# Performance work log

Hardware: AMD Instinct MI355X
Metric: run time of the kernel (lower is better)

Reference implementation:

```python
import jax, jax.numpy as jnp
import numpy as np

N_NODES = 50000
N_EDGES = 625000
IN_DIM = 512
HID = 128
OUT_DIM = 40
N_LAYERS = 3


def setup_inputs() -> dict:
    key = jax.random.key(0)
    ks = jax.random.split(key, 12)
    features = jax.random.normal(ks[0], (N_NODES, IN_DIM), dtype=jnp.float32)
    src = jax.random.randint(ks[1], (N_EDGES,), 0, N_NODES, dtype=jnp.int32)
    dst = jax.random.randint(ks[2], (N_EDGES,), 0, N_NODES, dtype=jnp.int32)
    edge_w = jax.random.uniform(ks[3], (N_EDGES,), dtype=jnp.float32)
    s_in = 1.0 / np.sqrt(IN_DIM)
    s_h = 1.0 / np.sqrt(HID)
    emb_W = jax.random.uniform(ks[4], (IN_DIM, HID), jnp.float32, -s_in, s_in)
    emb_b = jax.random.uniform(ks[5], (HID,), jnp.float32, -s_in, s_in)
    W1 = jax.random.uniform(ks[6], (N_LAYERS, HID, HID), jnp.float32, -s_h, s_h)
    b1 = jax.random.uniform(ks[7], (N_LAYERS, HID), jnp.float32, -s_h, s_h)
    W2 = jax.random.uniform(ks[8], (N_LAYERS, HID, HID), jnp.float32, -s_h, s_h)
    b2 = jax.random.uniform(ks[9], (N_LAYERS, HID), jnp.float32, -s_h, s_h)
    ro_W = jax.random.uniform(ks[10], (HID, OUT_DIM), jnp.float32, -s_h, s_h)
    ro_b = jax.random.uniform(ks[11], (OUT_DIM,), jnp.float32, -s_h, s_h)
    return {"features": features, "src": src, "dst": dst, "edge_w": edge_w,
            "emb_W": emb_W, "emb_b": emb_b, "W1": W1, "b1": b1,
            "W2": W2, "b2": b2, "ro_W": ro_W, "ro_b": ro_b}


def reference(features, src, dst, edge_w, emb_W, emb_b, W1, b1, W2, b2, ro_W, ro_b):
    # Input embedding: [N, in_dim] -> [N, hid]
    h = features @ emb_W + emb_b
    n = h.shape[0]
    for l in range(N_LAYERS):
        # GINConv (sum aggregator, eps=0): agg_i = sum_{(u->i)} w * h_u
        msg = h[src] * edge_w[:, None]                      # [E, hid]
        agg = jax.ops.segment_sum(msg, dst, num_segments=n)  # [N, hid]
        z = h + agg                                          # (1+eps)*h + agg
        # apply_func MLP: Linear -> ReLU -> Linear, then outer ReLU
        z = jax.nn.relu(z @ W1[l] + b1[l]) @ W2[l] + b2[l]
        h = jax.nn.relu(z)
    return h @ ro_W + ro_b
```

## Files before the change

### kernel.cpp

```cpp
#include <hip/hip_runtime.h>

#define NN 50000
#define NE 625000
#define IND 512
#define HID 128
#define OUTD 40
#define NL 3
#define NB 196

typedef short v8s __attribute__((ext_vector_type(8)));
typedef float v4f __attribute__((ext_vector_type(4)));
typedef const __attribute__((address_space(1))) unsigned int gu32;
typedef __attribute__((address_space(3))) unsigned int lu32;

#define MFMA __builtin_amdgcn_mfma_f32_16x16x32_bf16

__device__ inline ushort f2bf(float x) {
    unsigned u = __float_as_uint(x);
    u += 0x7FFF + ((u >> 16) & 1);
    return (ushort)(u >> 16);
}
__device__ inline float bf2f(ushort b) { return __uint_as_float(((unsigned)b) << 16); }

__device__ inline void split8(float4 a, float4 b, v8s& hi, v8s& lo) {
    float v[8] = {a.x, a.y, a.z, a.w, b.x, b.y, b.z, b.w};
    v8s h, l;
#pragma unroll
    for (int i = 0; i < 8; i++) {
        ushort hu = f2bf(v[i]);
        h[i] = (short)hu;
        l[i] = (short)f2bf(v[i] - bf2f(hu));
    }
    hi = h;
    lo = l;
}

template <int NI>
__device__ inline void stage(const ushort* __restrict__ g, ushort* l, int tid) {
    const int wid = tid >> 6;
#pragma unroll
    for (int j = 0; j < NI; j++) {
        __builtin_amdgcn_global_load_lds(
            (gu32*)((const char*)g + (size_t)(j * 256 + tid) * 16),
            (lu32*)((char*)l + (j * 256 + (wid << 6)) * 16), 16, 0, 0);
    }
}


__global__ __launch_bounds__(256) void count_kernel(const int* __restrict__ dst,
                                                    int* __restrict__ deg) {
    int e = blockIdx.x * 256 + threadIdx.x;
    if (e < NE) atomicAdd(&deg[dst[e]], 1);
}

__global__ __launch_bounds__(256) void scan1(const int* __restrict__ deg,
                                             int* __restrict__ ex,
                                             int* __restrict__ bsum) {
    __shared__ int s[256];
    int t = threadIdx.x;
    int idx = blockIdx.x * 256 + t;
    int d = idx < NN ? deg[idx] : 0;
    s[t] = d;
    __syncthreads();
#pragma unroll
    for (int off = 1; off < 256; off <<= 1) {
        int v = (t >= off) ? s[t - off] : 0;
        __syncthreads();
        s[t] += v;
        __syncthreads();
    }
    if (idx < NN) ex[idx] = s[t] - d;
    if (t == 255) bsum[blockIdx.x] = s[255];
}

__global__ __launch_bounds__(256) void scan2(const int* __restrict__ bsum,
                                             int* __restrict__ bpre) {
    __shared__ int s[256];
    int t = threadIdx.x;
    int d = t < NB ? bsum[t] : 0;
    s[t] = d;
    __syncthreads();
#pragma unroll
    for (int off = 1; off < 256; off <<= 1) {
        int v = (t >= off) ? s[t - off] : 0;
        __syncthreads();
        s[t] += v;
        __syncthreads();
    }
    if (t < NB) bpre[t] = s[t] - d;
}

__global__ __launch_bounds__(256) void scan3(const int* __restrict__ deg,
                                             const int* __restrict__ ex,
                                             const int* __restrict__ bpre,
                                             int* __restrict__ rp,
                                             int* __restrict__ cursor) {
    int idx = blockIdx.x * 256 + threadIdx.x;
    if (idx < NN) {
        int v = ex[idx] + bpre[blockIdx.x];
        rp[idx] = v;
        cursor[idx] = v;
        if (idx == NN - 1) rp[NN] = v + deg[idx];
    }
}

__global__ __launch_bounds__(256) void fill_kernel(const int* __restrict__ src,
                                                   const int* __restrict__ dst,
                                                   const float* __restrict__ ew,
                                                   int* __restrict__ cursor,
                                                   int2* __restrict__ csr) {
    int e = blockIdx.x * 256 + threadIdx.x;
    if (e < NE) {
        int d = dst[e];
        int pos = atomicAdd(&cursor[d], 1);
        csr[pos] = make_int2(src[e], __float_as_int(ew[e]));
    }
}


__global__ __launch_bounds__(256) void conv_emb(const float* __restrict__ W,
                                                ushort* __restrict__ P) {
    int idx = blockIdx.x * 256 + threadIdx.x;
    int k = idx >> 7;
    int c = idx & 127;
    float v = W[(size_t)k * HID + c];
    ushort hb = f2bf(v);
    ushort lb = f2bf(v - bf2f(hb));
    int it = k >> 6, kl = k & 63;
    int pos = it * 16384 + c * 64 + (kl ^ ((c & 7) << 3));
    P[pos] = hb;
    P[pos + 8192] = lb;
}

__global__ __launch_bounds__(256) void conv_mlp(const float* __restrict__ W1,
                                                const float* __restrict__ W2,
                                                ushort* __restrict__ P) {
    int idx = blockIdx.x * 256 + threadIdx.x;
    int lg = idx >> 14;
    int r = idx & 16383;
    int k = r >> 7, c = r & 127;
    int l = lg >> 1, g = lg & 1;
    const float* src = (g ? W2 : W1) + (size_t)l * HID * HID;
    float v = src[(size_t)k * HID + c];
    ushort hb = f2bf(v);
    ushort lb = f2bf(v - bf2f(hb));
    int q = c >> 5, cl = c & 31;
    int pos = lg * 32768 + q * 8192 + cl * 128 + (k ^ ((c & 7) << 3));
    P[pos] = hb;
    P[pos + 4096] = lb;
}

__global__ __launch_bounds__(256) void conv_ro(const float* __restrict__ W,
                                               ushort* __restrict__ Th,
                                               ushort* __restrict__ Tl) {
    int idx = blockIdx.x * 256 + threadIdx.x;
    int c = idx >> 7;
    int kk = idx & 127;
    float v = (c < OUTD) ? W[(size_t)kk * OUTD + c] : 0.f;
    ushort h = f2bf(v);
    Th[idx] = h;
    Tl[idx] = f2bf(v - bf2f(h));
}


__global__ __launch_bounds__(256) void emb_mfma(const float* __restrict__ X,
                                                const ushort* __restrict__ Wp,
                                                const float* __restrict__ B,
                                                float* __restrict__ H) {
    __shared__ __align__(16) ushort Wb[2][16384];
    const int tid = threadIdx.x;
    const int wid = tid >> 6, lane = tid & 63;
    const int lane15 = lane & 15, kg = (lane >> 4) * 8;
    const int swc = (lane15 & 7) << 3;
    const int brow = blockIdx.x * 64;
    const int grow = brow + wid * 16 + lane15;
    const float* xr = X + (size_t)(grow < NN ? grow : 0) * IND + kg;

    v4f acc[8];
#pragma unroll
    for (int i = 0; i < 8; i++) acc[i] = (v4f)0.f;

    float4 x0 = *reinterpret_cast<const float4*>(xr);
    float4 x1 = *reinterpret_cast<const float4*>(xr + 4);
    float4 x2 = *reinterpret_cast<const float4*>(xr + 32);
    float4 x3 = *reinterpret_cast<const float4*>(xr + 36);
    stage<8>(Wp, &Wb[0][0], tid);

    for (int it = 0; it < 8; ++it) {
        float4 n0, n1, n2, n3;
        if (it < 7) {
            const float* xn = xr + (it + 1) * 64;
            n0 = *reinterpret_cast<const float4*>(xn);
            n1 = *reinterpret_cast<const float4*>(xn + 4);
            n2 = *reinterpret_cast<const float4*>(xn + 32);
            n3 = *reinterpret_cast<const float4*>(xn + 36);
            stage<8>(Wp + (size_t)(it + 1) * 16384, &Wb[(it + 1) & 1][0], tid);
            asm volatile("s_waitcnt vmcnt(12)" ::: "memory");
        } else {
            asm volatile("s_waitcnt vmcnt(0)" ::: "memory");
        }
        __builtin_amdgcn_s_barrier();
        v8s ah0, al0, ah1, al1;
        split8(x0, x1, ah0, al0);
        split8(x2, x3, ah1, al1);
        const ushort* cb = &Wb[it & 1][0];
        const int s0 = kg ^ swc;
        const int s1 = (32 + kg) ^ swc;
        __builtin_amdgcn_s_setprio(1);
#pragma unroll
        for (int nf = 0; nf < 8; nf++) {
            int rb = (nf * 16 + lane15) * 64;
            v8s bh0 = *reinterpret_cast<const v8s*>(&cb[rb + s0]);
            v8s bl0 = *reinterpret_cast<const v8s*>(&cb[8192 + rb + s0]);
            v8s bh1 = *reinterpret_cast<const v8s*>(&cb[rb + s1]);
            v8s bl1 = *reinterpret_cast<const v8s*>(&cb[8192 + rb + s1]);
            v4f a = acc[nf];
            a = MFMA(ah0, bh0, a, 0, 0, 0);
            a = MFMA(al0, bh0, a, 0, 0, 0);
            a = MFMA(ah0, bl0, a, 0, 0, 0);
            a = MFMA(ah1, bh1, a, 0, 0, 0);
            a = MFMA(al1, bh1, a, 0, 0, 0);
            a = MFMA(ah1, bl1, a, 0, 0, 0);
            acc[nf] = a;
        }
        __builtin_amdgcn_s_setprio(0);
        asm volatile("s_waitcnt lgkmcnt(0)" ::: "memory");
        __builtin_amdgcn_s_barrier();
        x0 = n0; x1 = n1; x2 = n2; x3 = n3;
    }
#pragma unroll
    for (int nf = 0; nf < 8; nf++) {
        int col = nf * 16 + lane15;
        float bias = B[col];
#pragma unroll
        for (int r = 0; r < 4; r++) {
            int g = brow + wid * 16 + (lane >> 4) * 4 + r;
            if (g < NN) H[(size_t)g * HID + col] = acc[nf][r] + bias;
        }
    }
}


__global__ __launch_bounds__(256) void agg_kernel(const float* __restrict__ h,
                                                  const int* __restrict__ rp,
                                                  const int2* __restrict__ csr,
                                                  float* __restrict__ z) {
    const int node = blockIdx.x * 8 + (threadIdx.x >> 5);
    const int c4 = (threadIdx.x & 31) << 2;
    const float* hp = h + c4;
    v4f a0 = *reinterpret_cast<const v4f*>(hp + (size_t)node * HID);
    v4f a1 = (v4f)0.f, a2 = (v4f)0.f, a3 = (v4f)0.f;
    int k = rp[node];
    const int ke = rp[node + 1];
    for (; k + 3 < ke; k += 4) {
        int2 e0 = csr[k], e1 = csr[k + 1], e2 = csr[k + 2], e3 = csr[k + 3];
        a0 += __int_as_float(e0.y) * *reinterpret_cast<const v4f*>(hp + (size_t)e0.x * HID);
        a1 += __int_as_float(e1.y) * *reinterpret_cast<const v4f*>(hp + (size_t)e1.x * HID);
        a2 += __int_as_float(e2.y) * *reinterpret_cast<const v4f*>(hp + (size_t)e2.x * HID);
        a3 += __int_as_float(e3.y) * *reinterpret_cast<const v4f*>(hp + (size_t)e3.x * HID);
    }
    for (; k < ke; k++) {
        int2 e = csr[k];
        a0 += __int_as_float(e.y) * *reinterpret_cast<const v4f*>(hp + (size_t)e.x * HID);
    }
    *reinterpret_cast<v4f*>(z + (size_t)node * HID + c4) = (a0 + a1) + (a2 + a3);
}


template <int LAST>
__global__ __launch_bounds__(256) void mlp_mfma(const float* __restrict__ Z,
                                                const ushort* __restrict__ Wlp,
                                                const float* __restrict__ B1,
                                                const float* __restrict__ B2,
                                                const ushort* __restrict__ RWh,
                                                const ushort* __restrict__ RWl,
                                                const float* __restrict__ RB,
                                                float* __restrict__ H,
                                                float* __restrict__ OUT) {
    __shared__ __align__(16) ushort Wb[2][8192];
    __shared__ __align__(16) ushort Hh[64 * 128];
    __shared__ __align__(16) ushort Hl[64 * 128];
    const int tid = threadIdx.x;
    const int wid = tid >> 6, lane = tid & 63;
    const int lane15 = lane & 15, kg = (lane >> 4) * 8;
    const int swc = (lane15 & 7) << 3;
    const int brow = blockIdx.x * 64;
    const int grow = brow + wid * 16 + lane15;
    const int rowl = wid * 16 + lane15;
    const int sw = (rowl & 7) << 3;

    const float* zr = Z + (size_t)(grow < NN ? grow : 0) * HID + kg;
    float4 za[4], zb[4];
#pragma unroll
    for (int ks = 0; ks < 4; ks++) {
        za[ks] = *reinterpret_cast<const float4*>(zr + ks * 32);
        zb[ks] = *reinterpret_cast<const float4*>(zr + ks * 32 + 4);
    }
    stage<4>(Wlp, &Wb[0][0], tid);

    v8s ah[4], al[4];
    v4f acc[8];
#pragma unroll
    for (int i = 0; i < 8; i++) acc[i] = (v4f)0.f;

    for (int q = 0; q < 8; q++) {
        if (q < 7) {
            stage<4>(Wlp + (size_t)(q + 1) * 8192, &Wb[(q + 1) & 1][0], tid);
            asm volatile("s_waitcnt vmcnt(4)" ::: "memory");
        } else {
            asm volatile("s_waitcnt vmcnt(0)" ::: "memory");
        }
        __builtin_amdgcn_s_barrier();
        if (q == 0) {
#pragma unroll
            for (int ks = 0; ks < 4; ks++) split8(za[ks], zb[ks], ah[ks], al[ks]);
        }
        if (q == 4) {
#pragma unroll
            for (int ks = 0; ks < 4; ks++) {
                int idx = rowl * 128 + ((ks * 32 + kg) ^ sw);
                ah[ks] = *reinterpret_cast<const v8s*>(&Hh[idx]);
                al[ks] = *reinterpret_cast<const v8s*>(&Hl[idx]);
            }
        }
        const ushort* cb = &Wb[q & 1][0];
        const int nfb = (q & 3) * 2;
        __builtin_amdgcn_s_setprio(1);
#pragma unroll
        for (int t = 0; t < 2; t++) {
            int rb = (t * 16 + lane15) * 128;
            v4f a = acc[nfb + t];
#pragma unroll
            for (int ks = 0; ks < 4; ks++) {
                int s = (ks * 32 + kg) ^ swc;
                v8s bh = *reinterpret_cast<const v8s*>(&cb[rb + s]);
                v8s bl = *reinterpret_cast<const v8s*>(&cb[4096 + rb + s]);
                a = MFMA(ah[ks], bh, a, 0, 0, 0);
                a = MFMA(al[ks], bh, a, 0, 0, 0);
                a = MFMA(ah[ks], bl, a, 0, 0, 0);
            }
            acc[nfb + t] = a;
        }
        __builtin_amdgcn_s_setprio(0);
        if (q < 4) {
#pragma unroll
            for (int t = 0; t < 2; t++) {
                int nf = nfb + t;
                int col = nf * 16 + lane15;
                float b = B1[col];
#pragma unroll
                for (int r = 0; r < 4; r++) {
                    int rl2 = wid * 16 + (lane >> 4) * 4 + r;
                    float v = acc[nf][r] + b;
                    v = v > 0.f ? v : 0.f;
                    ushort hb = f2bf(v);
                    int idx = rl2 * 128 + (col ^ ((rl2 & 7) << 3));
                    Hh[idx] = hb;
                    Hl[idx] = f2bf(v - bf2f(hb));
                }
                acc[nf] = (v4f)0.f;
            }
        } else if (LAST == 0) {
#pragma unroll
            for (int t = 0; t < 2; t++) {
                int nf = nfb + t;
                int col = nf * 16 + lane15;
                float b = B2[col];
#pragma unroll
                for (int r = 0; r < 4; r++) {
                    int g = brow + wid * 16 + (lane >> 4) * 4 + r;
                    if (g < NN) H[(size_t)g * HID + col] = fmaxf(acc[nf][r] + b, 0.f);
                }
            }
        } else {
#pragma unroll
            for (int t = 0; t < 2; t++) {
                int nf = nfb + t;
                int col = nf * 16 + lane15;
                float b = B2[col];
#pragma unroll
                for (int r = 0; r < 4; r++) {
                    int rl2 = wid * 16 + (lane >> 4) * 4 + r;
                    float v = fmaxf(acc[nf][r] + b, 0.f);
                    ushort hb = f2bf(v);
                    int idx = rl2 * 128 + (col ^ ((rl2 & 7) << 3));
                    Hh[idx] = hb;
                    Hl[idx] = f2bf(v - bf2f(hb));
                }
            }
        }
        asm volatile("s_waitcnt lgkmcnt(0)" ::: "memory");
        __builtin_amdgcn_s_barrier();
    }

    if (LAST) {
#pragma unroll
        for (int ks = 0; ks < 4; ks++) {
            int idx = rowl * 128 + ((ks * 32 + kg) ^ sw);
            ah[ks] = *reinterpret_cast<const v8s*>(&Hh[idx]);
            al[ks] = *reinterpret_cast<const v8s*>(&Hl[idx]);
        }
        v4f a3[3];
#pragma unroll
        for (int i = 0; i < 3; i++) a3[i] = (v4f)0.f;
#pragma unroll
        for (int nf = 0; nf < 3; nf++) {
            const ushort* bp = RWh + (size_t)(nf * 16 + lane15) * HID + kg;
            const ushort* bq = RWl + (size_t)(nf * 16 + lane15) * HID + kg;
            v4f a = a3[nf];
#pragma unroll
            for (int ks = 0; ks < 4; ks++) {
                v8s bh = *reinterpret_cast<const v8s*>(bp + ks * 32);
                v8s bl = *reinterpret_cast<const v8s*>(bq + ks * 32);
                a = MFMA(ah[ks], bh, a, 0, 0, 0);
                a = MFMA(al[ks], bh, a, 0, 0, 0);
                a = MFMA(ah[ks], bl, a, 0, 0, 0);
            }
            a3[nf] = a;
        }
#pragma unroll
        for (int nf = 0; nf < 3; nf++) {
            int col = nf * 16 + lane15;
            if (col < OUTD) {
                float b = RB[col];
#pragma unroll
                for (int r = 0; r < 4; r++) {
                    int g = brow + wid * 16 + (lane >> 4) * 4 + r;
                    if (g < NN) OUT[(size_t)g * OUTD + col] = a3[nf][r] + b;
                }
            }
        }
    }
}


extern "C" void kernel_launch(void* const* d_in, const int* in_sizes, int n_in,
                              void* d_out, int out_size, void* d_ws, size_t ws_size,
                              hipStream_t stream) {
    const float* features = (const float*)d_in[0];
    const int* src = (const int*)d_in[1];
    const int* dst = (const int*)d_in[2];
    const float* ew = (const float*)d_in[3];
    const float* embW = (const float*)d_in[4];
    const float* embB = (const float*)d_in[5];
    const float* W1 = (const float*)d_in[6];
    const float* B1 = (const float*)d_in[7];
    const float* W2 = (const float*)d_in[8];
    const float* B2 = (const float*)d_in[9];
    const float* roW = (const float*)d_in[10];
    const float* roB = (const float*)d_in[11];
    float* out = (float*)d_out;

    float* h = (float*)d_ws;
    float* z = h + (size_t)NN * HID;
    int* rp = (int*)(z + (size_t)NN * HID);
    int2* csr = (int2*)(rp + NN + 16);
    int* cursor = (int*)(csr + NE);
    int* deg = cursor + NN;
    int* ex = deg + NN;
    int* bsum = ex + NN;
    int* bpre = bsum + NB + 4;
    ushort* Wemb_p = (ushort*)(bpre + NB + 4);
    ushort* Wmlp_p = Wemb_p + 8 * 16384;
    ushort* roWt_h = Wmlp_p + (size_t)NL * 8 * 8192;
    ushort* roWt_l = roWt_h + 48 * 128;

    conv_emb<<<256, 256, 0, stream>>>(embW, Wemb_p);
    conv_mlp<<<384, 256, 0, stream>>>(W1, W2, Wmlp_p);
    conv_ro<<<24, 256, 0, stream>>>(roW, roWt_h, roWt_l);

    hipMemsetAsync(deg, 0, NN * sizeof(int), stream);
    count_kernel<<<(NE + 255) / 256, 256, 0, stream>>>(dst, deg);
    scan1<<<NB, 256, 0, stream>>>(deg, ex, bsum);
    scan2<<<1, 256, 0, stream>>>(bsum, bpre);
    scan3<<<NB, 256, 0, stream>>>(deg, ex, bpre, rp, cursor);
    fill_kernel<<<(NE + 255) / 256, 256, 0, stream>>>(src, dst, ew, cursor, csr);

    emb_mfma<<<(NN + 63) / 64, 256, 0, stream>>>(features, Wemb_p, embB, h);

    for (int l = 0; l < NL; l++) {
        agg_kernel<<<NN / 8, 256, 0, stream>>>(h, rp, csr, z);
        const ushort* wl = Wmlp_p + (size_t)l * 8 * 8192;
        const float* b1 = B1 + (size_t)l * HID;
        const float* b2 = B2 + (size_t)l * HID;
        if (l < NL - 1) {
            mlp_mfma<0><<<(NN + 63) / 64, 256, 0, stream>>>(
                z, wl, b1, b2, roWt_h, roWt_l, roB, h, out);
        } else {
            mlp_mfma<1><<<(NN + 63) / 64, 256, 0, stream>>>(
                z, wl, b1, b2, roWt_h, roWt_l, roB, h, out);
        }
    }
}
```

Baseline: 539.8 us.

## Enlarge embedding blocks, triple-buffer MLP weights, unroll aggregation gathers by eight

The embedding GEMM now runs 512-thread blocks covering 128 rows, so each staged weight tile is shared by twice as many rows and fewer loads go out per thread. The MLP kernel moves from double to triple buffering of weight chunks, prefetching two stages ahead, and fully unrolls the stage loop. The aggregation loop issues eight neighbor gathers before accumulating, to expose more memory parallelism. The trade is more LDS per block in the MLP, larger blocks in the embedding, and higher register pressure in aggregation, all of which can lower occupancy.

```diff
diff --git a/kernel.cpp b/kernel.cpp
--- a/kernel.cpp
+++ b/kernel.cpp
@@ -35,14 +35,14 @@
     lo = l;
 }
 
-template <int NI>
+template <int NI, int NT>
 __device__ inline void stage(const ushort* __restrict__ g, ushort* l, int tid) {
-    const int wid = tid >> 6;
+    const int wbase = tid & ~63;
 #pragma unroll
     for (int j = 0; j < NI; j++) {
         __builtin_amdgcn_global_load_lds(
-            (gu32*)((const char*)g + (size_t)(j * 256 + tid) * 16),
-            (lu32*)((char*)l + (j * 256 + (wid << 6)) * 16), 16, 0, 0);
+            (gu32*)((const char*)g + (size_t)(j * NT + tid) * 16),
+            (lu32*)((char*)l + (j * NT + wbase) * 16), 16, 0, 0);
     }
 }
 
@@ -163,7 +163,7 @@
 }
 
 
-__global__ __launch_bounds__(256) void emb_mfma(const float* __restrict__ X,
+__global__ __launch_bounds__(512) void emb_mfma(const float* __restrict__ X,
                                                 const ushort* __restrict__ Wp,
                                                 const float* __restrict__ B,
                                                 float* __restrict__ H) {
@@ -172,7 +172,7 @@
     const int wid = tid >> 6, lane = tid & 63;
     const int lane15 = lane & 15, kg = (lane >> 4) * 8;
     const int swc = (lane15 & 7) << 3;
-    const int brow = blockIdx.x * 64;
+    const int brow = blockIdx.x * 128;
     const int grow = brow + wid * 16 + lane15;
     const float* xr = X + (size_t)(grow < NN ? grow : 0) * IND + kg;
 
@@ -184,7 +184,7 @@
     float4 x1 = *reinterpret_cast<const float4*>(xr + 4);
     float4 x2 = *reinterpret_cast<const float4*>(xr + 32);
     float4 x3 = *reinterpret_cast<const float4*>(xr + 36);
-    stage<8>(Wp, &Wb[0][0], tid);
+    stage<4, 512>(Wp, &Wb[0][0], tid);
 
     for (int it = 0; it < 8; ++it) {
         float4 n0, n1, n2, n3;
@@ -194,8 +194,8 @@
             n1 = *reinterpret_cast<const float4*>(xn + 4);
             n2 = *reinterpret_cast<const float4*>(xn + 32);
             n3 = *reinterpret_cast<const float4*>(xn + 36);
-            stage<8>(Wp + (size_t)(it + 1) * 16384, &Wb[(it + 1) & 1][0], tid);
-            asm volatile("s_waitcnt vmcnt(12)" ::: "memory");
+            stage<4, 512>(Wp + (size_t)(it + 1) * 16384, &Wb[(it + 1) & 1][0], tid);
+            asm volatile("s_waitcnt vmcnt(8)" ::: "memory");
         } else {
             asm volatile("s_waitcnt vmcnt(0)" ::: "memory");
         }
@@ -252,14 +252,32 @@
     v4f a1 = (v4f)0.f, a2 = (v4f)0.f, a3 = (v4f)0.f;
     int k = rp[node];
     const int ke = rp[node + 1];
-    for (; k + 3 < ke; k += 4) {
+    for (; k + 7 < ke; k += 8) {
         int2 e0 = csr[k], e1 = csr[k + 1], e2 = csr[k + 2], e3 = csr[k + 3];
+        int2 e4 = csr[k + 4], e5 = csr[k + 5], e6 = csr[k + 6], e7 = csr[k + 7];
+        const v4f v0 = *reinterpret_cast<const v4f*>(hp + (size_t)e0.x * HID);
+        const v4f v1 = *reinterpret_cast<const v4f*>(hp + (size_t)e1.x * HID);
+        const v4f v2 = *reinterpret_cast<const v4f*>(hp + (size_t)e2.x * HID);
+        const v4f v3 = *reinterpret_cast<const v4f*>(hp + (size_t)e3.x * HID);
+        const v4f v4 = *reinterpret_cast<const v4f*>(hp + (size_t)e4.x * HID);
+        const v4f v5 = *reinterpret_cast<const v4f*>(hp + (size_t)e5.x * HID);
+        const v4f v6 = *reinterpret_cast<const v4f*>(hp + (size_t)e6.x * HID);
+        const v4f v7 = *reinterpret_cast<const v4f*>(hp + (size_t)e7.x * HID);
+        a0 += __int_as_float(e0.y) * v0;
+        a1 += __int_as_float(e1.y) * v1;
+        a2 += __int_as_float(e2.y) * v2;
+        a3 += __int_as_float(e3.y) * v3;
+        a0 += __int_as_float(e4.y) * v4;
+        a1 += __int_as_float(e5.y) * v5;
+        a2 += __int_as_float(e6.y) * v6;
+        a3 += __int_as_float(e7.y) * v7;
+    }
+    for (; k + 1 < ke; k += 2) {
+        int2 e0 = csr[k], e1 = csr[k + 1];
         a0 += __int_as_float(e0.y) * *reinterpret_cast<const v4f*>(hp + (size_t)e0.x * HID);
         a1 += __int_as_float(e1.y) * *reinterpret_cast<const v4f*>(hp + (size_t)e1.x * HID);
-        a2 += __int_as_float(e2.y) * *reinterpret_cast<const v4f*>(hp + (size_t)e2.x * HID);
-        a3 += __int_as_float(e3.y) * *reinterpret_cast<const v4f*>(hp + (size_t)e3.x * HID);
-    }
-    for (; k < ke; k++) {
+    }
+    if (k < ke) {
         int2 e = csr[k];
         a0 += __int_as_float(e.y) * *reinterpret_cast<const v4f*>(hp + (size_t)e.x * HID);
     }
@@ -277,7 +295,7 @@
                                                 const float* __restrict__ RB,
                                                 float* __restrict__ H,
                                                 float* __restrict__ OUT) {
-    __shared__ __align__(16) ushort Wb[2][8192];
+    __shared__ __align__(16) ushort Wb[3][8192];
     __shared__ __align__(16) ushort Hh[64 * 128];
     __shared__ __align__(16) ushort Hl[64 * 128];
     const int tid = threadIdx.x;
@@ -296,16 +314,20 @@
         za[ks] = *reinterpret_cast<const float4*>(zr + ks * 32);
         zb[ks] = *reinterpret_cast<const float4*>(zr + ks * 32 + 4);
     }
-    stage<4>(Wlp, &Wb[0][0], tid);
+    stage<4, 256>(Wlp, &Wb[0][0], tid);
+    stage<4, 256>(Wlp + 8192, &Wb[1][0], tid);
 
     v8s ah[4], al[4];
     v4f acc[8];
 #pragma unroll
     for (int i = 0; i < 8; i++) acc[i] = (v4f)0.f;
 
+#pragma unroll
     for (int q = 0; q < 8; q++) {
-        if (q < 7) {
-            stage<4>(Wlp + (size_t)(q + 1) * 8192, &Wb[(q + 1) & 1][0], tid);
+        if (q < 6) {
+            stage<4, 256>(Wlp + (size_t)(q + 2) * 8192, &Wb[(q + 2) % 3][0], tid);
+            asm volatile("s_waitcnt vmcnt(8)" ::: "memory");
+        } else if (q == 6) {
             asm volatile("s_waitcnt vmcnt(4)" ::: "memory");
         } else {
             asm volatile("s_waitcnt vmcnt(0)" ::: "memory");
@@ -323,7 +345,7 @@
                 al[ks] = *reinterpret_cast<const v8s*>(&Hl[idx]);
             }
         }
-        const ushort* cb = &Wb[q & 1][0];
+        const ushort* cb = &Wb[q % 3][0];
         const int nfb = (q & 3) * 2;
         __builtin_amdgcn_s_setprio(1);
 #pragma unroll
@@ -476,7 +498,7 @@
     scan3<<<NB, 256, 0, stream>>>(deg, ex, bpre, rp, cursor);
     fill_kernel<<<(NE + 255) / 256, 256, 0, stream>>>(src, dst, ew, cursor, csr);
 
-    emb_mfma<<<(NN + 63) / 64, 256, 0, stream>>>(features, Wemb_p, embB, h);
+    emb_mfma<<<(NN + 127) / 128, 512, 0, stream>>>(features, Wemb_p, embB, h);
 
     for (int l = 0; l < NL; l++) {
         agg_kernel<<<NN / 8, 256, 0, stream>>>(h, rp, csr, z);
```

Measured after the change: 512.4 us. 5.1% less time.
